# Kernel tuning notes

Hardware: AMD Instinct MI355X
Metric: run time of the kernel (lower is better)

## Reference

```python
import jax, jax.numpy as jnp
import numpy as np
from jax import lax

H = W = 200          # feature map size
STRIDE = 16
IMG_H = IMG_W = H * STRIDE  # 3200
C = 512
A = 9                # 3 scales x 3 aspect ratios
K_PRE = 1000         # pre-NMS topk (hardcoded in module)
K_POST = 100         # post-NMS keep (hardcoded in module)
IOU_TH = 0.7


def make_anchors():
    scales = jnp.array([128.0, 256.0, 512.0], dtype=jnp.float32)
    ratios = jnp.array([0.5, 1.0, 2.0], dtype=jnp.float32)
    hr = jnp.sqrt(ratios)                      # (3,)
    wr = 1.0 / hr
    ws = (wr[:, None] * scales[None, :]).reshape(-1)   # (9,)
    hs = (hr[:, None] * scales[None, :]).reshape(-1)
    base = jnp.stack([-ws / 2, -hs / 2, ws / 2, hs / 2], axis=1)  # (9,4)
    sx = jnp.arange(W, dtype=jnp.float32) * STRIDE
    sy = jnp.arange(H, dtype=jnp.float32) * STRIDE
    gy, gx = jnp.meshgrid(sy, sx, indexing='ij')
    shifts = jnp.stack([gx, gy, gx, gy], axis=-1).reshape(-1, 4)  # (H*W,4)
    return (shifts[:, None, :] + base[None, :, :]).reshape(-1, 4)  # (H*W*A,4)


def decode(anchors, deltas):
    w = anchors[:, 2] - anchors[:, 0]
    h = anchors[:, 3] - anchors[:, 1]
    cx = anchors[:, 0] + 0.5 * w
    cy = anchors[:, 1] + 0.5 * h
    px = deltas[:, 0] * w + cx
    py = deltas[:, 1] * h + cy
    pw = jnp.exp(deltas[:, 2]) * w
    ph = jnp.exp(deltas[:, 3]) * h
    return jnp.stack([px - 0.5 * pw, py - 0.5 * ph, px + 0.5 * pw, py + 0.5 * ph], axis=1)


def clamp_boxes(b):
    return jnp.stack([
        jnp.clip(b[:, 0], 0.0, IMG_W), jnp.clip(b[:, 1], 0.0, IMG_H),
        jnp.clip(b[:, 2], 0.0, IMG_W), jnp.clip(b[:, 3], 0.0, IMG_H)], axis=1)


def nms_keep(boxes, thr):
    # boxes (K_PRE,4) already sorted by descending score (topk output order)
    x1, y1, x2, y2 = boxes[:, 0], boxes[:, 1], boxes[:, 2], boxes[:, 3]
    areas = (x2 - x1) * (y2 - y1)
    idx = jnp.arange(K_PRE)

    def body(i, keep):
        iw = jnp.clip(jnp.minimum(x2[i], x2) - jnp.maximum(x1[i], x1), 0.0)
        ih = jnp.clip(jnp.minimum(y2[i], y2) - jnp.maximum(y1[i], y1), 0.0)
        inter = iw * ih
        iou = inter / (areas[i] + areas - inter)
        supp = (iou > thr) & (idx > i) & keep[i]
        return keep & jnp.logical_not(supp)

    return lax.fori_loop(0, K_PRE, body, jnp.ones(K_PRE, dtype=bool))


def rpn_forward(feat, conv_w, conv_b, cls_w, cls_b, reg_w, reg_b):
    dn = ('NCHW', 'OIHW', 'NCHW')
    x = lax.conv_general_dilated(feat, conv_w, (1, 1), 'SAME', dimension_numbers=dn)
    x = jax.nn.relu(x + conv_b[None, :, None, None])
    cls = lax.conv_general_dilated(x, cls_w, (1, 1), 'SAME', dimension_numbers=dn) + cls_b[None, :, None, None]
    reg = lax.conv_general_dilated(x, reg_w, (1, 1), 'SAME', dimension_numbers=dn) + reg_b[None, :, None, None]
    # (1,A,H,W) -> (H*W*A,)
    cls_logits = cls.transpose(0, 2, 3, 1).reshape(-1)
    # (1,A*4,H,W) -> (H*W*A,4)
    deltas = reg.reshape(1, A, 4, H, W).transpose(0, 3, 4, 1, 2).reshape(-1, 4)
    anchors = make_anchors()
    proposals = decode(anchors, deltas)
    scores = jax.nn.sigmoid(cls_logits)
    top_sc, top_idx = lax.top_k(scores, K_PRE)           # sorted descending
    props = clamp_boxes(proposals[top_idx])
    keep = lax.stop_gradient(nms_keep(props, IOU_TH))    # NMS decision is non-diff
    # kept indices, in score order (stable sort puts kept first, preserving order)
    order = jnp.argsort(jnp.where(keep, 0, 1), stable=True)[:K_POST]
    valid = jnp.arange(K_POST) < jnp.sum(keep)
    out_boxes = jnp.where(valid[:, None], props[order], 0.0)
    out_scores = jnp.where(valid, top_sc[order], 0.0)
    return out_boxes, out_scores


def setup_inputs() -> dict:
    key = jax.random.key(0)
    ks = jax.random.split(key, 7)
    s = 0.02
    return {
        'feat': jax.random.normal(ks[0], (1, C, H, W), dtype=jnp.float32),
        'conv_w': jax.random.normal(ks[1], (C, C, 3, 3), dtype=jnp.float32) * s,
        'conv_b': jnp.zeros((C,), dtype=jnp.float32),
        'cls_w': jax.random.normal(ks[2], (A, C, 1, 1), dtype=jnp.float32) * s,
        'cls_b': jnp.zeros((A,), dtype=jnp.float32),
        'reg_w': jax.random.normal(ks[3], (A * 4, C, 1, 1), dtype=jnp.float32) * s,
        'reg_b': jnp.zeros((A * 4,), dtype=jnp.float32),
    }


def reference(feat, conv_w, conv_b, cls_w, cls_b, reg_w, reg_b):
    return rpn_forward(feat, conv_w, conv_b, cls_w, cls_b, reg_w, reg_b)
```

## Files before the change

kernel.cpp:

```cpp
#include <hip/hip_runtime.h>
#include <stdint.h>

static constexpr int H_ = 200, W_ = 200, HW_ = 40000;
static constexpr int C_ = 512;
static constexpr int NANCH = 360000;
static constexpr int KPRE = 1000;
static constexpr int KPOST = 100;
static constexpr int KSEL = 1400;
static constexpr int PXCAP = 4096;
static constexpr int KSPLIT = 8;
static constexpr int FT = 212;
static constexpr int FP = 202;

typedef __attribute__((ext_vector_type(8))) short bf16x8;
typedef __attribute__((ext_vector_type(4))) float f32x4;

__device__ inline ushort f2bf(float f) {
    unsigned u = __float_as_uint(f);
    u += 0x7FFFu + ((u >> 16) & 1u);
    return (ushort)(u >> 16);
}
__device__ inline float bf2f(ushort h) { return __uint_as_float(((unsigned)h) << 16); }

typedef const __attribute__((address_space(1))) uint32_t gas_u32;
typedef __attribute__((address_space(3))) uint32_t las_u32;
__device__ __forceinline__ void gload_lds16(const void* g, void* l) {
    __builtin_amdgcn_global_load_lds((gas_u32*)(uintptr_t)g, (las_u32*)(uintptr_t)l, 16, 0, 0);
}

__global__ void k_zero_u32(unsigned* __restrict__ p, int n) {
    int i = blockIdx.x * 256 + threadIdx.x;
    if (i < n) p[i] = 0u;
}

__global__ void k_zero_border_t(ushort* __restrict__ feat_t) {
    int t = blockIdx.x * 256 + threadIdx.x;
    int total = 4944 * 64;
    if (t >= total) return;
    int px = t >> 6, part = t & 63;
    int y, x;
    if (px < 2544) { int ri = px / 212; x = px - ri * 212; y = (ri == 0) ? 0 : 200 + ri; }
    else { int q = px - 2544; int r12 = q / 12; int c = q - r12 * 12; y = 1 + r12; x = (c == 0) ? 0 : 200 + c; }
    uint4 z = {0u, 0u, 0u, 0u};
    *(uint4*)&feat_t[((size_t)y * FT + x) * 512 + part * 8] = z;
}

__global__ void k_zero_border_px(float* __restrict__ feat_px) {
    int t = blockIdx.x * 256 + threadIdx.x;
    int total = 804 * 128;
    if (t >= total) return;
    int px = t >> 7, part = t & 127;
    int y, x;
    if (px < 202)      { y = 0;   x = px; }
    else if (px < 404) { y = 201; x = px - 202; }
    else if (px < 604) { x = 0;   y = 1 + (px - 404); }
    else               { x = 201; y = 1 + (px - 604); }
    float4 z = {0.f, 0.f, 0.f, 0.f};
    *(float4*)&feat_px[((size_t)y * FP + x) * 512 + part * 4] = z;
}

__global__ void k_feat_t(const float* __restrict__ feat, ushort* __restrict__ feat_t) {
    __shared__ ushort lt[32 * 8 * 33];
    int x0 = blockIdx.x * 32, y0 = blockIdx.y * 8, ci0 = blockIdx.z * 32;
    int tid = threadIdx.x;
    for (int u = tid; u < 8192; u += 256) {
        int ciL = u >> 8, rem = u & 255;
        int yy = rem >> 5, xx = rem & 31;
        int x = x0 + xx;
        float v = (x < W_) ? feat[(size_t)(ci0 + ciL) * HW_ + (y0 + yy) * W_ + x] : 0.f;
        lt[(ciL * 8 + yy) * 33 + xx] = f2bf(v);
    }
    __syncthreads();
    for (int u = tid; u < 1024; u += 256) {
        int pxu = u >> 2, part = u & 3;
        int yy = pxu >> 5, xx = pxu & 31;
        if (x0 + xx >= W_) continue;
        ushort tmp[8];
#pragma unroll
        for (int k = 0; k < 8; ++k) tmp[k] = lt[((part * 8 + k) * 8 + yy) * 33 + xx];
        *(uint4*)&feat_t[((size_t)(y0 + yy + 1) * FT + (x0 + xx + 1)) * 512 + ci0 + part * 8] =
            *(const uint4*)&tmp[0];
    }
}

__global__ void k_feat_px(const float* __restrict__ feat, float* __restrict__ feat_px) {
    __shared__ float lt[32 * 8 * 33];
    int x0 = blockIdx.x * 32, y0 = blockIdx.y * 8, ci0 = blockIdx.z * 32;
    int tid = threadIdx.x;
    for (int u = tid; u < 8192; u += 256) {
        int ciL = u >> 8, rem = u & 255;
        int yy = rem >> 5, xx = rem & 31;
        int x = x0 + xx;
        float v = (x < W_) ? feat[(size_t)(ci0 + ciL) * HW_ + (y0 + yy) * W_ + x] : 0.f;
        lt[(ciL * 8 + yy) * 33 + xx] = v;
    }
    __syncthreads();
    for (int u = tid; u < 1024; u += 256) {
        int pxu = u >> 2, part = u & 3;
        int yy = pxu >> 5, xx = pxu & 31;
        if (x0 + xx >= W_) continue;
        float tmp[8];
#pragma unroll
        for (int k = 0; k < 8; ++k) tmp[k] = lt[((part * 8 + k) * 8 + yy) * 33 + xx];
        float* dst = &feat_px[((size_t)(y0 + yy + 1) * FP + (x0 + xx + 1)) * 512 + ci0 + part * 8];
        *(float4*)&dst[0] = *(const float4*)&tmp[0];
        *(float4*)&dst[4] = *(const float4*)&tmp[4];
    }
}

__global__ void k_wt_t(const float* __restrict__ conv_w, ushort* __restrict__ wt_t) {
    int i = blockIdx.x * 256 + threadIdx.x;
    if (i >= 9 * 512 * 512) return;
    int tap = i >> 18;
    int rem = i & 262143;
    int co = rem >> 9, ci = rem & 511;
    wt_t[i] = f2bf(conv_w[((size_t)co * 512 + ci) * 9 + tap]);
}

__global__ void k_wt_ex(const float* __restrict__ conv_w, float* __restrict__ wt_ex) {
    __shared__ float t[32][33];
    int kb = blockIdx.x * 32;
    int cb = blockIdx.y * 32;
    int lx = threadIdx.x, ly = threadIdx.y;
    int tap = kb >> 9, ci0 = kb & 511;
    for (int r = ly; r < 32; r += 8)
        t[r][lx] = conv_w[((size_t)(cb + r) * 512 + ci0 + lx) * 9 + tap];
    __syncthreads();
    for (int r = ly; r < 32; r += 8)
        wt_ex[(size_t)(kb + r) * 512 + cb + lx] = t[lx][r];
}

__global__ __launch_bounds__(256)
__attribute__((amdgpu_waves_per_eu(2, 4)))
void k_conv3_mfma(const ushort* __restrict__ feat_t, const ushort* __restrict__ wt_t,
                  const float* __restrict__ bias, ushort* __restrict__ xab) {
    __shared__ ushort halo[18 * 34 * 32];
    __shared__ ushort wtile[9 * 64 * 32];
    int b = blockIdx.x;
    int cot = b & 7;
    int tile = b >> 3;
    int xt = tile % 7, yt = tile / 7;
    int x0 = xt * 32, y0 = yt * 16;
    int co0 = cot * 64;
    int tid = threadIdx.x;
    int lane = tid & 63, wid = tid >> 6;
    int l15 = lane & 15, l4 = lane >> 4;

    f32x4 acc[4][2][4];
#pragma unroll
    for (int i = 0; i < 4; ++i)
#pragma unroll
        for (int h = 0; h < 2; ++h)
#pragma unroll
            for (int j = 0; j < 4; ++j) acc[i][h][j] = (f32x4){0.f, 0.f, 0.f, 0.f};

    for (int ch = 0; ch < 16; ++ch) {
        int ci0 = ch * 32;
        __syncthreads();
        for (int u = tid; u < 2448; u += 256) {
            int p = u >> 2, q = u & 3;
            int r = p / 34, c = p - r * 34;
            const ushort* src = feat_t + ((size_t)(y0 + r) * FT + (x0 + c)) * 512 + ci0 + q * 8;
            gload_lds16(src, &halo[(u & ~63) * 8]);
        }
        for (int u = tid; u < 2304; u += 256) {
            int row = u >> 2, q = u & 3;
            int tap = row >> 6, co = row & 63;
            const ushort* src = wt_t + ((size_t)(tap * 512 + co0 + co)) * 512 + ci0 + q * 8;
            gload_lds16(src, &wtile[(u & ~63) * 8]);
        }
        __syncthreads();
#pragma unroll
        for (int tap = 0; tap < 9; ++tap) {
            int th = tap / 3, tw = tap - th * 3;
            bf16x8 af[4][2];
#pragma unroll
            for (int pi = 0; pi < 4; ++pi)
#pragma unroll
                for (int xh = 0; xh < 2; ++xh)
                    af[pi][xh] = *(const bf16x8*)&halo[
                        ((wid * 4 + pi + th) * 34 + (xh * 16 + l15 + tw)) * 32 + l4 * 8];
#pragma unroll
            for (int cj = 0; cj < 4; ++cj) {
                bf16x8 bf = *(const bf16x8*)&wtile[(tap * 64 + cj * 16 + l15) * 32 + l4 * 8];
#pragma unroll
                for (int pi = 0; pi < 4; ++pi)
#pragma unroll
                    for (int xh = 0; xh < 2; ++xh)
                        acc[pi][xh][cj] = __builtin_amdgcn_mfma_f32_16x16x32_bf16(
                            af[pi][xh], bf, acc[pi][xh][cj], 0, 0, 0);
            }
        }
    }

    float bv[4];
#pragma unroll
    for (int cj = 0; cj < 4; ++cj) bv[cj] = bias[co0 + cj * 16 + l15];
#pragma unroll
    for (int pi = 0; pi < 4; ++pi) {
        int yy = y0 + wid * 4 + pi;
        if (yy >= H_) continue;
#pragma unroll
        for (int xh = 0; xh < 2; ++xh) {
#pragma unroll
            for (int cj = 0; cj < 4; ++cj) {
                int co = co0 + cj * 16 + l15;
#pragma unroll
                for (int r = 0; r < 4; ++r) {
                    int xx = x0 + xh * 16 + l4 * 4 + r;
                    if (xx < W_) {
                        float v = acc[pi][xh][cj][r] + bv[cj];
                        xab[((size_t)(yy * W_ + xx)) * 512 + co] = f2bf(v > 0.f ? v : 0.f);
                    }
                }
            }
        }
    }
}

__global__ void k_cls(const ushort* __restrict__ xab, const float* __restrict__ cls_w,
                      const float* __restrict__ cls_b, float* __restrict__ scores) {
    __shared__ ushort xt[64 * 520];
    int t = threadIdx.x;
    int pxb = blockIdx.x * 64;
    for (int i = 0; i < 64; ++i)
        *(uint4*)&xt[i * 520 + t * 8] =
            *(const uint4*)&xab[((size_t)(pxb + i)) * 512 + t * 8];
    __syncthreads();
    float acc[9];
#pragma unroll
    for (int a = 0; a < 9; ++a) acc[a] = 0.f;
    const ushort* row = &xt[t * 520];
    for (int k = 0; k < 64; ++k) {
        bf16x8 v = *(const bf16x8*)&row[k * 8];
        float xv[8];
#pragma unroll
        for (int j = 0; j < 8; ++j) xv[j] = bf2f((ushort)v[j]);
#pragma unroll
        for (int a = 0; a < 9; ++a)
#pragma unroll
            for (int j = 0; j < 8; ++j)
                acc[a] = fmaf(xv[j], cls_w[a * 512 + k * 8 + j], acc[a]);
    }
    int px = pxb + t;
#pragma unroll
    for (int a = 0; a < 9; ++a)
        scores[(size_t)px * 9 + a] = 1.f / (1.f + expf(-(acc[a] + cls_b[a])));
}

__global__ void k_hist1_lds(const float* __restrict__ scores, unsigned* __restrict__ hist) {
    __shared__ unsigned h[16384];
    int tid = threadIdx.x;
    for (int j = tid; j < 16384; j += 256) h[j] = 0u;
    __syncthreads();
    int stride = gridDim.x * 256;
    for (int i = blockIdx.x * 256 + tid; i < NANCH; i += stride)
        atomicAdd(&h[(__float_as_uint(scores[i]) >> 16) & 16383], 1u);
    __syncthreads();
    for (int j = tid; j < 16384; j += 256) {
        unsigned v = h[j];
        if (v) atomicAdd(&hist[j], v);
    }
}

__global__ void k_find_thr(const unsigned* __restrict__ hist, unsigned* __restrict__ meta,
                           int mode, int Kwant) {
    __shared__ unsigned csum[1024];
    int t = threadIdx.x;
    unsigned base = (mode == 0) ? 0u : meta[1];
    unsigned s = 0;
    for (int b = 0; b < 64; ++b) s += hist[t * 64 + b];
    csum[t] = s;
    __syncthreads();
    for (int off = 1; off < 1024; off <<= 1) {
        unsigned add = (t + off < 1024) ? csum[t + off] : 0u;
        __syncthreads();
        csum[t] += add;
        __syncthreads();
    }
    unsigned run = base + ((t < 1023) ? csum[t + 1] : 0u);
    for (int b = 63; b >= 0; --b) {
        unsigned h = hist[t * 64 + b];
        if (run < (unsigned)Kwant && run + h >= (unsigned)Kwant) {
            if (mode == 0) {
                meta[0] = (unsigned)(t * 64 + b);
                meta[1] = run;
            } else {
                meta[2] = (meta[0] << 16) | (unsigned)(t * 64 + b);
                meta[3] = run;
                meta[4] = (unsigned)Kwant - run;
            }
            break;
        }
        run += h;
    }
}

__global__ void k_collect_cand(const float* __restrict__ scores, const unsigned* __restrict__ meta,
                               unsigned* __restrict__ flags) {
    int i = blockIdx.x * 256 + threadIdx.x;
    if (i >= NANCH) return;
    if ((__float_as_uint(scores[i]) >> 16) >= meta[0]) flags[i / 9] = 1u;
}

__global__ void k_px_compact(unsigned* __restrict__ flags, unsigned* __restrict__ meta,
                             unsigned* __restrict__ px_list) {
    int px = blockIdx.x * 256 + threadIdx.x;
    if (px >= HW_) return;
    if (flags[px]) {
        unsigned s = atomicAdd(&meta[10], 1u);
        if (s < (unsigned)PXCAP) { px_list[s] = (unsigned)px; flags[px] = s + 1u; }
        else flags[px] = 0u;
    }
}

__global__ __attribute__((amdgpu_waves_per_eu(2, 4)))
void k_exact_gemm(const float* __restrict__ feat_px, const float* __restrict__ wt_ex,
                  const unsigned* __restrict__ meta, const unsigned* __restrict__ px_list,
                  float* __restrict__ xpart) {
    int npx = (int)meta[10]; if (npx > PXCAP) npx = PXCAP;
    int pb = blockIdx.x;
    if (pb * 64 >= npx) return;
    int cot = blockIdx.y;
    int kz = blockIdx.z;
    __shared__ float A[32][68];
    __shared__ float B[32][68];
    __shared__ int plist[64];
    int tid = threadIdx.x;
    int co0 = cot * 64;
    if (tid < 64) {
        int slot = pb * 64 + tid;
        plist[tid] = (slot < npx) ? (int)px_list[slot] : (int)px_list[0];
    }
    int tcog = tid >> 4;
    int tpxg = tid & 15;
    float acc[4][4];
#pragma unroll
    for (int i = 0; i < 4; ++i)
#pragma unroll
        for (int j = 0; j < 4; ++j) acc[i][j] = 0.f;
    int kbase = kz * 576;
    for (int kc = 0; kc < 18; ++kc) {
        int k0 = kbase + kc * 32;
        int tap = k0 >> 9, ci0c = k0 & 511;
        int th = tap / 3, tw = tap - th * 3;
        __syncthreads();
        for (int u = tid; u < 512; u += 256) {
            int k = u >> 4, cp = (u & 15) * 4;
            *(float4*)&A[k][cp] = *(const float4*)&wt_ex[(size_t)(k0 + k) * 512 + co0 + cp];
        }
        for (int u = tid; u < 512; u += 256) {
            int s = u >> 3, part = u & 7;
            int px = plist[s];
            int y = px / W_, x = px - y * W_;
            float4 v = *(const float4*)&feat_px[((size_t)(y + th) * FP + (x + tw)) * 512 + ci0c + part * 4];
            B[part * 4 + 0][s] = v.x; B[part * 4 + 1][s] = v.y;
            B[part * 4 + 2][s] = v.z; B[part * 4 + 3][s] = v.w;
        }
        __syncthreads();
#pragma unroll 4
        for (int k = 0; k < 32; ++k) {
            float wv[4], pv[4];
            *(float4*)&wv[0] = *(const float4*)&A[k][tcog * 4];
            *(float4*)&pv[0] = *(const float4*)&B[k][tpxg * 4];
#pragma unroll
            for (int i = 0; i < 4; ++i)
#pragma unroll
                for (int j = 0; j < 4; ++j) acc[i][j] = fmaf(wv[i], pv[j], acc[i][j]);
        }
    }
#pragma unroll
    for (int j = 0; j < 4; ++j) {
        int slot = pb * 64 + tpxg * 4 + j;
        if (slot >= npx) continue;
        f32x4 tmp;
        tmp[0] = acc[0][j]; tmp[1] = acc[1][j]; tmp[2] = acc[2][j]; tmp[3] = acc[3][j];
        __builtin_nontemporal_store(tmp,
            (f32x4*)&xpart[((size_t)kz * PXCAP + slot) * 512 + co0 + tcog * 4]);
    }
}

__global__ void k_exact_reduce(const float* __restrict__ xpart, const float* __restrict__ bias,
                               const unsigned* __restrict__ meta, float* __restrict__ xex) {
    int npx = (int)meta[10]; if (npx > PXCAP) npx = PXCAP;
    int idx = blockIdx.x * 256 + threadIdx.x;
    int slot = idx >> 9, co = idx & 511;
    if (slot >= npx) return;
    float v = 0.f;
#pragma unroll
    for (int kz = 0; kz < KSPLIT; ++kz)
        v += __builtin_nontemporal_load(&xpart[((size_t)kz * PXCAP + slot) * 512 + co]);
    v += bias[co];
    xex[(size_t)slot * 512 + co] = v > 0.f ? v : 0.f;
}

__global__ void k_exact_scores(const float* __restrict__ xex, const float* __restrict__ cls_w,
                               const float* __restrict__ cls_b, const unsigned* __restrict__ meta,
                               float* __restrict__ scores_ex) {
    int slot = blockIdx.x;
    int npx = (int)meta[10]; if (npx > PXCAP) npx = PXCAP;
    if (slot >= npx) return;
    int l = threadIdx.x;
    float xv[8];
#pragma unroll
    for (int k = 0; k < 8; ++k) xv[k] = xex[(size_t)slot * 512 + k * 64 + l];
#pragma unroll
    for (int a = 0; a < 9; ++a) {
        float s = 0.f;
#pragma unroll
        for (int k = 0; k < 8; ++k) s = fmaf(xv[k], cls_w[a * 512 + k * 64 + l], s);
#pragma unroll
        for (int o = 32; o > 0; o >>= 1) s += __shfl_down(s, o);
        if (l == 0) scores_ex[slot * 9 + a] = 1.f / (1.f + expf(-(s + cls_b[a])));
    }
}

__global__ void k_hist1_ex_lds(const float* __restrict__ scores_ex, const unsigned* __restrict__ meta,
                               unsigned* __restrict__ hist) {
    __shared__ unsigned h[16384];
    int npx = (int)meta[10]; if (npx > PXCAP) npx = PXCAP;
    int n = npx * 9;
    int tid = threadIdx.x;
    for (int j = tid; j < 16384; j += 256) h[j] = 0u;
    __syncthreads();
    for (int i = blockIdx.x * 256 + tid; i < n; i += 32 * 256)
        atomicAdd(&h[(__float_as_uint(scores_ex[i]) >> 16) & 16383], 1u);
    __syncthreads();
    for (int j = tid; j < 16384; j += 256) {
        unsigned v = h[j];
        if (v) atomicAdd(&hist[j], v);
    }
}

__global__ void k_hist2_ex(const float* __restrict__ scores_ex, const unsigned* __restrict__ meta,
                           const unsigned* __restrict__ meta_ex, unsigned* __restrict__ hist2) {
    int npx = (int)meta[10]; if (npx > PXCAP) npx = PXCAP;
    int i = blockIdx.x * 256 + threadIdx.x;
    if (i >= npx * 9) return;
    unsigned b = __float_as_uint(scores_ex[i]);
    if ((b >> 16) == meta_ex[0]) atomicAdd(&hist2[b & 0xFFFFu], 1u);
}

__global__ void k_collect_ex(const float* __restrict__ scores_ex, const unsigned* __restrict__ meta,
                             unsigned* __restrict__ meta_ex, const unsigned* __restrict__ px_list,
                             unsigned* __restrict__ sel_bits, unsigned* __restrict__ sel_idx,
                             unsigned* __restrict__ eq_idx) {
    int npx = (int)meta[10]; if (npx > PXCAP) npx = PXCAP;
    int i = blockIdx.x * 256 + threadIdx.x;
    if (i >= npx * 9) return;
    unsigned b = __float_as_uint(scores_ex[i]);
    unsigned T = meta_ex[2];
    unsigned g = px_list[i / 9] * 9u + (unsigned)(i % 9);
    if (b > T) {
        unsigned s = atomicAdd(&meta_ex[8], 1u);
        if (s < 1024u) { sel_bits[s] = b; sel_idx[s] = g; }
    } else if (b == T) {
        unsigned s = atomicAdd(&meta_ex[9], 1u);
        if (s < 65536u) eq_idx[s] = g;
    }
}

__global__ void k_topk_final(const unsigned* __restrict__ sel_bits, const unsigned* __restrict__ sel_idx,
                             const unsigned* __restrict__ eq_idx, const unsigned* __restrict__ meta,
                             unsigned* __restrict__ top_idx, float* __restrict__ top_sc) {
    __shared__ uint64_t keys[1024];
    __shared__ int lcnt;
    __shared__ int lred;
    int t = threadIdx.x;
    unsigned cntGt = meta[3];
    unsigned need = meta[4];
    unsigned cntEq = meta[9];
    unsigned T = meta[2];

    unsigned idx_cut = 0xFFFFFFFFu;
    if (cntEq > need) {
        unsigned lo = 0, hi = NANCH - 1;
        while (lo < hi) {
            unsigned mid = (lo + hi) >> 1;
            int c = 0;
            for (unsigned e = t; e < cntEq; e += 1024)
                if (eq_idx[e] <= mid) c++;
            if (t == 0) lred = 0;
            __syncthreads();
            atomicAdd(&lred, c);
            __syncthreads();
            int tot = lred;
            __syncthreads();
            if ((unsigned)tot >= need) hi = mid; else lo = mid + 1;
        }
        idx_cut = lo;
    }

    keys[t] = 0ull;
    if (t == 0) lcnt = 0;
    __syncthreads();
    for (unsigned s = t; s < cntGt; s += 1024)
        keys[s] = ((uint64_t)sel_bits[s] << 32) | (uint64_t)(0xFFFFFFFFu - sel_idx[s]);
    for (unsigned e = t; e < cntEq; e += 1024) {
        unsigned ix = eq_idx[e];
        if (ix <= idx_cut) {
            int s2 = (int)cntGt + atomicAdd(&lcnt, 1);
            keys[s2] = ((uint64_t)T << 32) | (uint64_t)(0xFFFFFFFFu - ix);
        }
    }
    __syncthreads();
    for (int k = 2; k <= 1024; k <<= 1) {
        for (int j = k >> 1; j > 0; j >>= 1) {
            int ixj = t ^ j;
            if (ixj > t) {
                uint64_t a = keys[t], b = keys[ixj];
                bool desc = (t & k) == 0;
                if (desc ? (a < b) : (a > b)) { keys[t] = b; keys[ixj] = a; }
            }
            __syncthreads();
        }
    }
    if (t < KPRE) {
        top_sc[t] = __uint_as_float((unsigned)(keys[t] >> 32));
        top_idx[t] = 0xFFFFFFFFu - (unsigned)keys[t];
    }
}

__global__ void k_decode(const float* __restrict__ xex, const unsigned* __restrict__ flags,
                         const float* __restrict__ reg_w, const float* __restrict__ reg_b,
                         const unsigned* __restrict__ top_idx,
                         float* __restrict__ props, float* __restrict__ areas) {
    int j = blockIdx.x;
    int lane = threadIdx.x;
    unsigned idx = top_idx[j];
    int pix = (int)(idx / 9u);
    int a = (int)(idx - (unsigned)pix * 9u);
    int slot = (int)flags[pix] - 1;
    if (slot < 0) slot = 0;
    const float* xr = xex + (size_t)slot * 512;
    float s0 = 0, s1 = 0, s2 = 0, s3 = 0;
    for (int c = lane; c < C_; c += 64) {
        float xv = xr[c];
        s0 = fmaf(xv, reg_w[(a * 4 + 0) * C_ + c], s0);
        s1 = fmaf(xv, reg_w[(a * 4 + 1) * C_ + c], s1);
        s2 = fmaf(xv, reg_w[(a * 4 + 2) * C_ + c], s2);
        s3 = fmaf(xv, reg_w[(a * 4 + 3) * C_ + c], s3);
    }
#pragma unroll
    for (int o = 32; o > 0; o >>= 1) {
        s0 += __shfl_down(s0, o);
        s1 += __shfl_down(s1, o);
        s2 += __shfl_down(s2, o);
        s3 += __shfl_down(s3, o);
    }
    if (lane == 0) {
        float d0 = s0 + reg_b[a * 4 + 0];
        float d1 = s1 + reg_b[a * 4 + 1];
        float d2 = s2 + reg_b[a * 4 + 2];
        float d3 = s3 + reg_b[a * 4 + 3];
        int h = pix / W_, w2 = pix - h * W_;
        int rr = a / 3, ss = a - rr * 3;
        float ratio = (rr == 0) ? 0.5f : (rr == 1) ? 1.0f : 2.0f;
        float scale = (ss == 0) ? 128.f : (ss == 1) ? 256.f : 512.f;
        float hr = sqrtf(ratio);
        float wr = 1.0f / hr;
        float wsc = wr * scale, hsc = hr * scale;
        float sx = (float)w2 * 16.f, sy = (float)h * 16.f;
        float a0 = sx - wsc * 0.5f, a1 = sy - hsc * 0.5f;
        float a2 = sx + wsc * 0.5f, a3 = sy + hsc * 0.5f;
        float bw = a2 - a0, bh = a3 - a1;
        float cx = a0 + 0.5f * bw, cy = a1 + 0.5f * bh;
        float px = d0 * bw + cx, py = d1 * bh + cy;
        float pw = expf(d2) * bw, ph = expf(d3) * bh;
        float b0 = px - 0.5f * pw, b1 = py - 0.5f * ph;
        float b2 = px + 0.5f * pw, b3 = py + 0.5f * ph;
        b0 = fminf(fmaxf(b0, 0.f), 3200.f);
        b1 = fminf(fmaxf(b1, 0.f), 3200.f);
        b2 = fminf(fmaxf(b2, 0.f), 3200.f);
        b3 = fminf(fmaxf(b3, 0.f), 3200.f);
        props[j * 4 + 0] = b0;
        props[j * 4 + 1] = b1;
        props[j * 4 + 2] = b2;
        props[j * 4 + 3] = b3;
        areas[j] = (b2 - b0) * (b3 - b1);
    }
}

__global__ void k_nms_mask(const float* __restrict__ props, const float* __restrict__ areas,
                           unsigned long long* __restrict__ mask, float* __restrict__ out) {
    int i = blockIdx.x;
    int tid = threadIdx.x;
    if (i == 0) {
        for (int t = tid; t < KPOST * 5; t += 256) out[t] = 0.f;
    }
    float x1i = props[i * 4 + 0], y1i = props[i * 4 + 1];
    float x2i = props[i * 4 + 2], y2i = props[i * 4 + 3];
    float ai = areas[i];
#pragma unroll
    for (int k = 0; k < 4; ++k) {
        int j = k * 256 + tid;
        bool sup = false;
        if (j < KPRE && j > i) {
            float iw = fminf(x2i, props[j * 4 + 2]) - fmaxf(x1i, props[j * 4 + 0]);
            float ih = fminf(y2i, props[j * 4 + 3]) - fmaxf(y1i, props[j * 4 + 1]);
            iw = fmaxf(iw, 0.f);
            ih = fmaxf(ih, 0.f);
            float inter = iw * ih;
            float iou = inter / (ai + areas[j] - inter);
            sup = iou > 0.7f;
        }
        unsigned long long b = __ballot(sup);
        int word = k * 4 + (tid >> 6);
        if ((tid & 63) == 0) mask[(size_t)i * 16 + word] = b;
    }
}

__global__ void k_nms_scan_out(const unsigned long long* __restrict__ mask,
                               const float* __restrict__ props, const float* __restrict__ top_sc,
                               float* __restrict__ out) {
    __shared__ int kidx[KPOST];
    __shared__ int nk;
    int lane = threadIdx.x;
    if (lane == 0) {
        unsigned long long k0 = ~0ull, k1 = ~0ull, k2 = ~0ull, k3 = ~0ull;
        unsigned long long k4 = ~0ull, k5 = ~0ull, k6 = ~0ull, k7 = ~0ull;
        unsigned long long k8 = ~0ull, k9 = ~0ull, k10 = ~0ull, k11 = ~0ull;
        unsigned long long k12 = ~0ull, k13 = ~0ull, k14 = ~0ull;
        unsigned long long k15 = (1ull << 40) - 1ull;
        int kept = 0;
#define APPLY_ROW(ii) { const unsigned long long* row = &mask[(size_t)(ii) * 16];          \
        k0 &= ~row[0];  k1 &= ~row[1];  k2 &= ~row[2];  k3 &= ~row[3];                     \
        k4 &= ~row[4];  k5 &= ~row[5];  k6 &= ~row[6];  k7 &= ~row[7];                     \
        k8 &= ~row[8];  k9 &= ~row[9];  k10 &= ~row[10]; k11 &= ~row[11];                  \
        k12 &= ~row[12]; k13 &= ~row[13]; k14 &= ~row[14]; k15 &= ~row[15]; }
#define SCAN_WORD(w, kw) { \
        unsigned long long rem = kw; \
        while (rem) { \
            int b = __builtin_ctzll(rem); \
            kidx[kept++] = (w) * 64 + b; \
            if (kept == KPOST) goto done; \
            APPLY_ROW((w) * 64 + b); \
            rem &= kw; \
            rem &= (b >= 63) ? 0ull : ~((2ull << b) - 1ull); \
        } }
        SCAN_WORD(0, k0)  SCAN_WORD(1, k1)  SCAN_WORD(2, k2)  SCAN_WORD(3, k3)
        SCAN_WORD(4, k4)  SCAN_WORD(5, k5)  SCAN_WORD(6, k6)  SCAN_WORD(7, k7)
        SCAN_WORD(8, k8)  SCAN_WORD(9, k9)  SCAN_WORD(10, k10) SCAN_WORD(11, k11)
        SCAN_WORD(12, k12) SCAN_WORD(13, k13) SCAN_WORD(14, k14) SCAN_WORD(15, k15)
done:
        nk = kept;
#undef SCAN_WORD
#undef APPLY_ROW
    }
    __syncthreads();
    int n = nk;
    for (int t = lane; t < KPOST; t += 64) {
        if (t < n) {
            int i = kidx[t];
            out[t * 4 + 0] = props[i * 4 + 0];
            out[t * 4 + 1] = props[i * 4 + 1];
            out[t * 4 + 2] = props[i * 4 + 2];
            out[t * 4 + 3] = props[i * 4 + 3];
            out[KPOST * 4 + t] = top_sc[i];
        }
    }
}

extern "C" void kernel_launch(void* const* d_in, const int* in_sizes, int n_in,
                              void* d_out, int out_size, void* d_ws, size_t ws_size,
                              hipStream_t stream) {
    const float* feat   = (const float*)d_in[0];
    const float* conv_w = (const float*)d_in[1];
    const float* conv_b = (const float*)d_in[2];
    const float* cls_w  = (const float*)d_in[3];
    const float* cls_b  = (const float*)d_in[4];
    const float* reg_w  = (const float*)d_in[5];
    const float* reg_b  = (const float*)d_in[6];
    float* out = (float*)d_out;

    size_t off = 0;
    auto alloc = [&](size_t bytes) -> void* {
        off = (off + 255) & ~(size_t)255;
        void* p = (char*)d_ws + off;
        off += bytes;
        return p;
    };
    ushort* feat_t  = (ushort*)alloc((size_t)FT * FT * 512 * 2);
    float*  feat_px = (float*)alloc((size_t)FP * FP * 512 * 4);
    ushort* wt_t    = (ushort*)alloc((size_t)9 * 512 * 512 * 2);
    float*  wt_ex   = (float*)alloc((size_t)9 * 512 * 512 * 4);
    ushort* xab     = (ushort*)alloc((size_t)HW_ * 512 * 2);
    float*  xpart   = (float*)alloc((size_t)KSPLIT * PXCAP * 512 * 4);
    float*  xex     = (float*)alloc((size_t)PXCAP * 512 * 4);
    float*  scores  = (float*)alloc((size_t)NANCH * 4);
    float*  scores_ex = (float*)alloc((size_t)PXCAP * 9 * 4);
    unsigned* hist1   = (unsigned*)alloc(65536 * 4);
    unsigned* hist2   = (unsigned*)alloc(65536 * 4);
    unsigned* meta    = (unsigned*)alloc(64 * 4);
    unsigned* meta_ex = (unsigned*)alloc(64 * 4);
    unsigned* flags   = (unsigned*)alloc((size_t)HW_ * 4);
    unsigned* px_list = (unsigned*)alloc(PXCAP * 4);
    unsigned* sel_bits = (unsigned*)alloc(1024 * 4);
    unsigned* sel_idx  = (unsigned*)alloc(1024 * 4);
    unsigned* eq_idx   = (unsigned*)alloc(65536 * 4);
    unsigned* top_idx  = (unsigned*)alloc(KPRE * 4);
    float* top_sc      = (float*)alloc(KPRE * 4);
    float* props       = (float*)alloc(KPRE * 4 * 4);
    float* areas       = (float*)alloc(KPRE * 4);
    unsigned long long* mask = (unsigned long long*)alloc((size_t)KPRE * 16 * 8);
    (void)ws_size; (void)in_sizes; (void)n_in; (void)out_size;

    k_zero_border_t<<<(4944 * 64 + 255) / 256, 256, 0, stream>>>(feat_t);
    int zrDw = 65536 * 2 + 64 + 64 + HW_;
    k_zero_u32<<<(zrDw + 255) / 256, 256, 0, stream>>>(hist1, zrDw);
    k_feat_t<<<dim3(7, 25, 16), 256, 0, stream>>>(feat, feat_t);
    k_wt_t<<<(9 * 512 * 512 + 255) / 256, 256, 0, stream>>>(conv_w, wt_t);
    k_conv3_mfma<<<8 * 91, 256, 0, stream>>>(feat_t, wt_t, conv_b, xab);
    k_cls<<<HW_ / 64, 64, 0, stream>>>(xab, cls_w, cls_b, scores);
    k_hist1_lds<<<64, 256, 0, stream>>>(scores, hist1);
    k_find_thr<<<1, 1024, 0, stream>>>(hist1, meta, 0, KSEL);
    k_collect_cand<<<(NANCH + 255) / 256, 256, 0, stream>>>(scores, meta, flags);
    k_px_compact<<<(HW_ + 255) / 256, 256, 0, stream>>>(flags, meta, px_list);
    k_zero_border_px<<<(804 * 128 + 255) / 256, 256, 0, stream>>>(feat_px);
    k_feat_px<<<dim3(7, 25, 16), 256, 0, stream>>>(feat, feat_px);
    k_wt_ex<<<dim3(144, 16), dim3(32, 8), 0, stream>>>(conv_w, wt_ex);
    k_zero_u32<<<(65536 * 2 + 255) / 256, 256, 0, stream>>>(hist1, 65536 * 2);
    k_exact_gemm<<<dim3(PXCAP / 64, 8, KSPLIT), 256, 0, stream>>>(feat_px, wt_ex, meta, px_list, xpart);
    k_exact_reduce<<<PXCAP * 512 / 256, 256, 0, stream>>>(xpart, conv_b, meta, xex);
    k_exact_scores<<<PXCAP, 64, 0, stream>>>(xex, cls_w, cls_b, meta, scores_ex);
    k_hist1_ex_lds<<<32, 256, 0, stream>>>(scores_ex, meta, hist1);
    k_find_thr<<<1, 1024, 0, stream>>>(hist1, meta_ex, 0, KPRE);
    k_hist2_ex<<<(PXCAP * 9 + 255) / 256, 256, 0, stream>>>(scores_ex, meta, meta_ex, hist2);
    k_find_thr<<<1, 1024, 0, stream>>>(hist2, meta_ex, 1, KPRE);
    k_collect_ex<<<(PXCAP * 9 + 255) / 256, 256, 0, stream>>>(scores_ex, meta, meta_ex, px_list,
                                                              sel_bits, sel_idx, eq_idx);
    k_topk_final<<<1, 1024, 0, stream>>>(sel_bits, sel_idx, eq_idx, meta_ex, top_idx, top_sc);
    k_decode<<<KPRE, 64, 0, stream>>>(xex, flags, reg_w, reg_b, top_idx, props, areas);
    k_nms_mask<<<KPRE, 256, 0, stream>>>(props, areas, mask, out);
    k_nms_scan_out<<<1, 64, 0, stream>>>(mask, props, top_sc, out);
}
```

Measured before the change: 705.8 us.

## Fuse weight transforms, exact reduce+scores, widen exact GEMM K-chunk, drop zero pass

Merges the two weight-layout kernels into one that reads conv_w once and writes both the bf16 and fp32 layouts. Fuses the split-K reduction with the classifier score kernel so the reduced activations stay in registers. Doubles the exact GEMM K-chunk to 64, halving barrier count at the cost of twice the shared memory. Gives the exact-path histograms their own buffers, cleared in the initial zero pass, which removes the mid-pipeline zero launch.

```diff
diff --git a/kernel.cpp b/kernel.cpp
--- a/kernel.cpp
+++ b/kernel.cpp
@@ -108,23 +108,18 @@
     }
 }
 
-__global__ void k_wt_t(const float* __restrict__ conv_w, ushort* __restrict__ wt_t) {
-    int i = blockIdx.x * 256 + threadIdx.x;
-    if (i >= 9 * 512 * 512) return;
-    int tap = i >> 18;
-    int rem = i & 262143;
-    int co = rem >> 9, ci = rem & 511;
-    wt_t[i] = f2bf(conv_w[((size_t)co * 512 + ci) * 9 + tap]);
-}
-
-__global__ void k_wt_ex(const float* __restrict__ conv_w, float* __restrict__ wt_ex) {
+__global__ void k_wt_both(const float* __restrict__ conv_w, ushort* __restrict__ wt_t,
+                          float* __restrict__ wt_ex) {
     __shared__ float t[32][33];
     int kb = blockIdx.x * 32;
     int cb = blockIdx.y * 32;
     int lx = threadIdx.x, ly = threadIdx.y;
     int tap = kb >> 9, ci0 = kb & 511;
-    for (int r = ly; r < 32; r += 8)
-        t[r][lx] = conv_w[((size_t)(cb + r) * 512 + ci0 + lx) * 9 + tap];
+    for (int r = ly; r < 32; r += 8) {
+        float v = conv_w[((size_t)(cb + r) * 512 + ci0 + lx) * 9 + tap];
+        t[r][lx] = v;
+        wt_t[(size_t)tap * 262144 + (size_t)(cb + r) * 512 + ci0 + lx] = f2bf(v);
+    }
     __syncthreads();
     for (int r = ly; r < 32; r += 8)
         wt_ex[(size_t)(kb + r) * 512 + cb + lx] = t[lx][r];
@@ -323,8 +318,8 @@
     if (pb * 64 >= npx) return;
     int cot = blockIdx.y;
     int kz = blockIdx.z;
-    __shared__ float A[32][68];
-    __shared__ float B[32][68];
+    __shared__ float A[64][68];
+    __shared__ float B[64][68];
     __shared__ int plist[64];
     int tid = threadIdx.x;
     int co0 = cot * 64;
@@ -340,26 +335,30 @@
 #pragma unroll
         for (int j = 0; j < 4; ++j) acc[i][j] = 0.f;
     int kbase = kz * 576;
-    for (int kc = 0; kc < 18; ++kc) {
-        int k0 = kbase + kc * 32;
-        int tap = k0 >> 9, ci0c = k0 & 511;
-        int th = tap / 3, tw = tap - th * 3;
+    for (int kc = 0; kc < 9; ++kc) {
+        int k0 = kbase + kc * 64;
         __syncthreads();
-        for (int u = tid; u < 512; u += 256) {
+        for (int u = tid; u < 1024; u += 256) {
             int k = u >> 4, cp = (u & 15) * 4;
             *(float4*)&A[k][cp] = *(const float4*)&wt_ex[(size_t)(k0 + k) * 512 + co0 + cp];
         }
-        for (int u = tid; u < 512; u += 256) {
-            int s = u >> 3, part = u & 7;
-            int px = plist[s];
-            int y = px / W_, x = px - y * W_;
-            float4 v = *(const float4*)&feat_px[((size_t)(y + th) * FP + (x + tw)) * 512 + ci0c + part * 4];
-            B[part * 4 + 0][s] = v.x; B[part * 4 + 1][s] = v.y;
-            B[part * 4 + 2][s] = v.z; B[part * 4 + 3][s] = v.w;
+#pragma unroll
+        for (int hh = 0; hh < 2; ++hh) {
+            int kh = k0 + hh * 32;
+            int tap = kh >> 9, ci0c = kh & 511;
+            int th = tap / 3, tw = tap - th * 3;
+            for (int u = tid; u < 512; u += 256) {
+                int s = u >> 3, part = u & 7;
+                int px = plist[s];
+                int y = px / W_, x = px - y * W_;
+                float4 v = *(const float4*)&feat_px[((size_t)(y + th) * FP + (x + tw)) * 512 + ci0c + part * 4];
+                B[hh * 32 + part * 4 + 0][s] = v.x; B[hh * 32 + part * 4 + 1][s] = v.y;
+                B[hh * 32 + part * 4 + 2][s] = v.z; B[hh * 32 + part * 4 + 3][s] = v.w;
+            }
         }
         __syncthreads();
 #pragma unroll 4
-        for (int k = 0; k < 32; ++k) {
+        for (int k = 0; k < 64; ++k) {
             float wv[4], pv[4];
             *(float4*)&wv[0] = *(const float4*)&A[k][tcog * 4];
             *(float4*)&pv[0] = *(const float4*)&B[k][tpxg * 4];
@@ -380,30 +379,27 @@
     }
 }
 
-__global__ void k_exact_reduce(const float* __restrict__ xpart, const float* __restrict__ bias,
-                               const unsigned* __restrict__ meta, float* __restrict__ xex) {
-    int npx = (int)meta[10]; if (npx > PXCAP) npx = PXCAP;
-    int idx = blockIdx.x * 256 + threadIdx.x;
-    int slot = idx >> 9, co = idx & 511;
-    if (slot >= npx) return;
-    float v = 0.f;
-#pragma unroll
-    for (int kz = 0; kz < KSPLIT; ++kz)
-        v += __builtin_nontemporal_load(&xpart[((size_t)kz * PXCAP + slot) * 512 + co]);
-    v += bias[co];
-    xex[(size_t)slot * 512 + co] = v > 0.f ? v : 0.f;
-}
-
-__global__ void k_exact_scores(const float* __restrict__ xex, const float* __restrict__ cls_w,
-                               const float* __restrict__ cls_b, const unsigned* __restrict__ meta,
-                               float* __restrict__ scores_ex) {
+__global__ void k_exact_fin(const float* __restrict__ xpart, const float* __restrict__ bias,
+                            const float* __restrict__ cls_w, const float* __restrict__ cls_b,
+                            const unsigned* __restrict__ meta,
+                            float* __restrict__ xex, float* __restrict__ scores_ex) {
     int slot = blockIdx.x;
     int npx = (int)meta[10]; if (npx > PXCAP) npx = PXCAP;
     if (slot >= npx) return;
     int l = threadIdx.x;
     float xv[8];
 #pragma unroll
-    for (int k = 0; k < 8; ++k) xv[k] = xex[(size_t)slot * 512 + k * 64 + l];
+    for (int j = 0; j < 8; ++j) {
+        int co = j * 64 + l;
+        float v = 0.f;
+#pragma unroll
+        for (int kz = 0; kz < KSPLIT; ++kz)
+            v += __builtin_nontemporal_load(&xpart[((size_t)kz * PXCAP + slot) * 512 + co]);
+        v += bias[co];
+        v = v > 0.f ? v : 0.f;
+        xex[(size_t)slot * 512 + co] = v;
+        xv[j] = v;
+    }
 #pragma unroll
     for (int a = 0; a < 9; ++a) {
         float s = 0.f;
@@ -691,6 +687,8 @@
     float*  scores_ex = (float*)alloc((size_t)PXCAP * 9 * 4);
     unsigned* hist1   = (unsigned*)alloc(65536 * 4);
     unsigned* hist2   = (unsigned*)alloc(65536 * 4);
+    unsigned* hist1e  = (unsigned*)alloc(65536 * 4);
+    unsigned* hist2e  = (unsigned*)alloc(65536 * 4);
     unsigned* meta    = (unsigned*)alloc(64 * 4);
     unsigned* meta_ex = (unsigned*)alloc(64 * 4);
     unsigned* flags   = (unsigned*)alloc((size_t)HW_ * 4);
@@ -706,10 +704,10 @@
     (void)ws_size; (void)in_sizes; (void)n_in; (void)out_size;
 
     k_zero_border_t<<<(4944 * 64 + 255) / 256, 256, 0, stream>>>(feat_t);
-    int zrDw = 65536 * 2 + 64 + 64 + HW_;
+    int zrDw = 65536 * 4 + 128 + HW_;
     k_zero_u32<<<(zrDw + 255) / 256, 256, 0, stream>>>(hist1, zrDw);
     k_feat_t<<<dim3(7, 25, 16), 256, 0, stream>>>(feat, feat_t);
-    k_wt_t<<<(9 * 512 * 512 + 255) / 256, 256, 0, stream>>>(conv_w, wt_t);
+    k_wt_both<<<dim3(144, 16), dim3(32, 8), 0, stream>>>(conv_w, wt_t, wt_ex);
     k_conv3_mfma<<<8 * 91, 256, 0, stream>>>(feat_t, wt_t, conv_b, xab);
     k_cls<<<HW_ / 64, 64, 0, stream>>>(xab, cls_w, cls_b, scores);
     k_hist1_lds<<<64, 256, 0, stream>>>(scores, hist1);
@@ -718,15 +716,12 @@
     k_px_compact<<<(HW_ + 255) / 256, 256, 0, stream>>>(flags, meta, px_list);
     k_zero_border_px<<<(804 * 128 + 255) / 256, 256, 0, stream>>>(feat_px);
     k_feat_px<<<dim3(7, 25, 16), 256, 0, stream>>>(feat, feat_px);
-    k_wt_ex<<<dim3(144, 16), dim3(32, 8), 0, stream>>>(conv_w, wt_ex);
-    k_zero_u32<<<(65536 * 2 + 255) / 256, 256, 0, stream>>>(hist1, 65536 * 2);
     k_exact_gemm<<<dim3(PXCAP / 64, 8, KSPLIT), 256, 0, stream>>>(feat_px, wt_ex, meta, px_list, xpart);
-    k_exact_reduce<<<PXCAP * 512 / 256, 256, 0, stream>>>(xpart, conv_b, meta, xex);
-    k_exact_scores<<<PXCAP, 64, 0, stream>>>(xex, cls_w, cls_b, meta, scores_ex);
-    k_hist1_ex_lds<<<32, 256, 0, stream>>>(scores_ex, meta, hist1);
-    k_find_thr<<<1, 1024, 0, stream>>>(hist1, meta_ex, 0, KPRE);
-    k_hist2_ex<<<(PXCAP * 9 + 255) / 256, 256, 0, stream>>>(scores_ex, meta, meta_ex, hist2);
-    k_find_thr<<<1, 1024, 0, stream>>>(hist2, meta_ex, 1, KPRE);
+    k_exact_fin<<<PXCAP, 64, 0, stream>>>(xpart, conv_b, cls_w, cls_b, meta, xex, scores_ex);
+    k_hist1_ex_lds<<<32, 256, 0, stream>>>(scores_ex, meta, hist1e);
+    k_find_thr<<<1, 1024, 0, stream>>>(hist1e, meta_ex, 0, KPRE);
+    k_hist2_ex<<<(PXCAP * 9 + 255) / 256, 256, 0, stream>>>(scores_ex, meta, meta_ex, hist2e);
+    k_find_thr<<<1, 1024, 0, stream>>>(hist2e, meta_ex, 1, KPRE);
     k_collect_ex<<<(PXCAP * 9 + 255) / 256, 256, 0, stream>>>(scores_ex, meta, meta_ex, px_list,
                                                               sel_bits, sel_idx, eq_idx);
     k_topk_final<<<1, 1024, 0, stream>>>(sel_bits, sel_idx, eq_idx, meta_ex, top_idx, top_sc);
```

Measured after the change: 709.7 us. Within noise of the previous version (+0.5%).
